# Kernel optimization log

Hardware: AMD Instinct MI355X
Metric: run time of the kernel (lower is better)

Reference implementation:

```python
import jax, jax.numpy as jnp
import numpy as np

FRAC_BITS = 16            # fixed-point fractional bits (MPC fixedpoint precision)
SCALE = float(1 << FRAC_BITS)

def fxp(v):
    """Emulate dup_with_precision: round value to the fixed-point grid with
    FRAC_BITS fractional bits. Straight-through (identity) gradient, matching
    the MPC backward pass which propagates gradients through truncation."""
    return v + jax.lax.stop_gradient(jnp.round(v * SCALE) / SCALE - v)


def setup_inputs() -> dict:
    key = jax.random.key(0)
    kx, kw = jax.random.split(key)
    in_dim, out_dim, batch = 4096, 4096, 2048
    x = jax.random.normal(kx, (batch, in_dim), dtype=jnp.float32)
    # Dense_Local init: w ~ N(0, 1/sqrt(in_dim+1)), b = zeros
    w = jax.random.normal(kw, (in_dim, out_dim), dtype=jnp.float32) / np.sqrt(in_dim + 1)
    b = jnp.zeros((out_dim,), dtype=jnp.float32)
    return {"x": x, "w": w, "b": b}


def reference(x, w, b):
    # quantize operands to the fixed-point grid (values live on the grid in MPC)
    xq = fxp(x)
    wq = fxp(w)
    # y = x @ w, then dup_with_precision(x.fixedpoint): truncate product back
    y = fxp(jnp.matmul(xq, wq))           # [batch, out_dim]
    # + bias
    y = y + fxp(b)
    # secure ReLU: s = drelu_local(y) (sign bit), y = relu(y, s) = y * s
    s = y >= 0
    y = jnp.where(s, y, jnp.zeros((), dtype=y.dtype))
    # final dup_with_precision(new_fixedpoint=x.fixedpoint)
    return fxp(y)
```

## Files before the change

kernel.cpp:

```cpp
#include <hip/hip_runtime.h>
#include <hip/hip_bf16.h>
#include <stdint.h>

#define M_DIM 2048
#define N_DIM 4096
#define K_DIM 4096

#define NT 64

typedef short short8 __attribute__((ext_vector_type(8)));
typedef float f32x4 __attribute__((ext_vector_type(4)));

typedef __attribute__((address_space(1))) unsigned int gu32;
typedef __attribute__((address_space(3))) unsigned int lu32;

__device__ static inline unsigned short f32_to_bf16(float f) {
  union { float f; unsigned int u; } v; v.f = f;
  unsigned int u = v.u;
  u += 0x7FFFu + ((u >> 16) & 1u);
  return (unsigned short)(u >> 16);
}

__global__ void cvt_x_kernel(const float* __restrict__ in, unsigned short* __restrict__ out) {
  size_t i = ((size_t)blockIdx.x * blockDim.x + threadIdx.x) * 8;
  f32x4 a = *(const f32x4*)(in + i);
  f32x4 b = *(const f32x4*)(in + i + 4);
  short8 o;
  o[0] = (short)f32_to_bf16(a[0]); o[1] = (short)f32_to_bf16(a[1]);
  o[2] = (short)f32_to_bf16(a[2]); o[3] = (short)f32_to_bf16(a[3]);
  o[4] = (short)f32_to_bf16(b[0]); o[5] = (short)f32_to_bf16(b[1]);
  o[6] = (short)f32_to_bf16(b[2]); o[7] = (short)f32_to_bf16(b[3]);
  *(short8*)(out + i) = o;
}

__global__ void transpose_cvt_w_kernel(const float* __restrict__ w, unsigned short* __restrict__ wt) {
  __shared__ unsigned short tile[64][64 + 8];
  int bn = blockIdx.x * 64;
  int bk = blockIdx.y * 64;
  int t = threadIdx.x;
  int c4 = (t & 15) * 4;
  int r0 = t >> 4;
#pragma unroll
  for (int p = 0; p < 4; ++p) {
    int r = r0 + p * 16;
    f32x4 v = *(const f32x4*)(w + (size_t)(bk + r) * N_DIM + bn + c4);
    tile[c4 + 0][r] = f32_to_bf16(v[0]);
    tile[c4 + 1][r] = f32_to_bf16(v[1]);
    tile[c4 + 2][r] = f32_to_bf16(v[2]);
    tile[c4 + 3][r] = f32_to_bf16(v[3]);
  }
  __syncthreads();
  int orow = t >> 2;
  int oc = (t & 3) * 16;
  short8 lo, hi;
#pragma unroll
  for (int j = 0; j < 8; ++j) {
    lo[j] = (short)tile[orow][oc + j];
    hi[j] = (short)tile[orow][oc + 8 + j];
  }
  unsigned short* op = wt + (size_t)(bn + orow) * K_DIM + bk + oc;
  *(short8*)(op) = lo;
  *(short8*)(op + 8) = hi;
}


__global__ __launch_bounds__(256, 1) void gemm4_kernel(
    const unsigned short* __restrict__ A, const unsigned short* __restrict__ Bt,
    const float* __restrict__ bias, float* __restrict__ C) {
  __shared__ unsigned short smA[3 * 24576];
  char* smemc = (char*)&smA[0];

  const int tid = threadIdx.x;
  const int lane = tid & 63;
  const int w = tid >> 6;
  const int wm = w >> 1, wn = w & 1;

  const int id = blockIdx.x;
  const int x = id & 7, j = id >> 3;
  const int by = ((x >> 2) << 3) + (j >> 2);
  const int bx = ((x & 3) << 2) + (j & 3);
  const int r0 = by * 128, c0 = bx * 256;

  const int l8 = lane >> 3, l7 = lane & 7;
  const int chunkE = ((l7 ^ l8) << 3);
  const unsigned short* Ag = A + (size_t)(r0 + w * 32 + l8) * K_DIM + chunkE;
  const unsigned short* Bg = Bt + (size_t)(c0 + w * 64 + l8) * K_DIM + chunkE;

#define GL(gp, ldsoff) __builtin_amdgcn_global_load_lds((gu32*)(gp), (lu32*)(smemc + (ldsoff)), 16, 0, 0)
  auto STAGE = [&](int T, int sb) {
#pragma unroll
    for (int i = 0; i < 4; ++i)
      GL(Ag + (size_t)T * 64 + (size_t)i * 8 * K_DIM, sb + w * 4096 + i * 1024);
#pragma unroll
    for (int i = 0; i < 8; ++i)
      GL(Bg + (size_t)T * 64 + (size_t)i * 8 * K_DIM, sb + 16384 + w * 8192 + i * 1024);
  };

  const int l15 = lane & 15, hi = lane >> 4;
  const int aR = (wm * 64 + l15) * 64;
  const int bR = 8192 + (wn * 128 + l15) * 64;
  const int slot0 = ((hi ^ l7) << 3);
  const int slot1 = (((4 + hi) ^ l7) << 3);

  f32x4 acc[4][8] = {};

  STAGE(0, 0);
  STAGE(1, 49152);

  int cs = 0;
  for (int t = 0; t < NT; ++t) {
    const int sE = cs * 24576;
    const int stB = (cs == 0 ? 2 : cs - 1) * 49152;

    if (t < NT - 1) asm volatile("s_waitcnt vmcnt(12) lgkmcnt(0)" ::: "memory");
    else            asm volatile("s_waitcnt vmcnt(0) lgkmcnt(0)" ::: "memory");
    __builtin_amdgcn_sched_barrier(0);
    asm volatile("s_barrier" ::: "memory");

    short8 a0[4], b0[8];
#pragma unroll
    for (int m = 0; m < 4; ++m) a0[m] = *(const short8*)(smA + sE + aR + m * 1024 + slot0);
#pragma unroll
    for (int n = 0; n < 8; ++n) b0[n] = *(const short8*)(smA + sE + bR + n * 1024 + slot0);
    if (t + 2 < NT) STAGE(t + 2, stB);

    __builtin_amdgcn_s_setprio(1);
#pragma unroll
    for (int m = 0; m < 4; ++m)
#pragma unroll
      for (int n = 0; n < 8; ++n)
        acc[m][n] = __builtin_amdgcn_mfma_f32_16x16x32_bf16(a0[m], b0[n], acc[m][n], 0, 0, 0);
    __builtin_amdgcn_s_setprio(0);

    short8 a1[4], b1[8];
#pragma unroll
    for (int m = 0; m < 4; ++m) a1[m] = *(const short8*)(smA + sE + aR + m * 1024 + slot1);
#pragma unroll
    for (int n = 0; n < 8; ++n) b1[n] = *(const short8*)(smA + sE + bR + n * 1024 + slot1);

    __builtin_amdgcn_s_setprio(1);
#pragma unroll
    for (int m = 0; m < 4; ++m)
#pragma unroll
      for (int n = 0; n < 8; ++n)
        acc[m][n] = __builtin_amdgcn_mfma_f32_16x16x32_bf16(a1[m], b1[n], acc[m][n], 0, 0, 0);
    __builtin_amdgcn_s_setprio(0);

    cs = (cs == 2) ? 0 : cs + 1;
  }

  const float S = 65536.0f, IS = 1.0f / 65536.0f;
  const int lr = hi * 4;
#pragma unroll
  for (int n = 0; n < 8; ++n) {
    int gcol = c0 + wn * 128 + n * 16 + l15;
    float bq = rintf(bias[gcol] * S) * IS;
#pragma unroll
    for (int m = 0; m < 4; ++m) {
      int grow = r0 + wm * 64 + m * 16 + lr;
      float* outp = C + (size_t)grow * N_DIM + gcol;
#pragma unroll
      for (int r = 0; r < 4; ++r) {
        float t = rintf(acc[m][n][r] * S) * IS + bq;
        t = t > 0.0f ? t : 0.0f;
        outp[(size_t)r * N_DIM] = t;
      }
    }
  }
#undef GL
}

__global__ __launch_bounds__(256, 2) void gemm_fb_kernel(
    const float* __restrict__ Xf, const float* __restrict__ Wf,
    const float* __restrict__ bias, float* __restrict__ C) {
  __shared__ unsigned short As[128][64];
  __shared__ unsigned short Bs[128][64];
  int tid = threadIdx.x;
  int lane = tid & 63;
  int wid = tid >> 6;
  int wr = wid >> 1, wc = wid & 1;
  int r0 = blockIdx.y * 128;
  int c0 = blockIdx.x * 128;
  f32x4 acc[4][4] = {};
  for (int kt = 0; kt < K_DIM / 64; ++kt) {
    __syncthreads();
    int ar = tid >> 1;
    int ac = (tid & 1) * 32;
    const float* xp = Xf + (size_t)(r0 + ar) * K_DIM + kt * 64 + ac;
#pragma unroll
    for (int jj = 0; jj < 8; ++jj) {
      f32x4 v = *(const f32x4*)(xp + jj * 4);
      As[ar][ac + jj * 4 + 0] = f32_to_bf16(v[0]);
      As[ar][ac + jj * 4 + 1] = f32_to_bf16(v[1]);
      As[ar][ac + jj * 4 + 2] = f32_to_bf16(v[2]);
      As[ar][ac + jj * 4 + 3] = f32_to_bf16(v[3]);
    }
    int bk_ = tid >> 2;
    int bc = (tid & 3) * 32;
    const float* wp = Wf + (size_t)(kt * 64 + bk_) * N_DIM + c0 + bc;
#pragma unroll
    for (int jj = 0; jj < 8; ++jj) {
      f32x4 v = *(const f32x4*)(wp + jj * 4);
      Bs[bc + jj * 4 + 0][bk_] = f32_to_bf16(v[0]);
      Bs[bc + jj * 4 + 1][bk_] = f32_to_bf16(v[1]);
      Bs[bc + jj * 4 + 2][bk_] = f32_to_bf16(v[2]);
      Bs[bc + jj * 4 + 3][bk_] = f32_to_bf16(v[3]);
    }
    __syncthreads();
#pragma unroll
    for (int ks = 0; ks < 2; ++ks) {
      int co = ks * 32 + (lane >> 4) * 8;
      int rA = wr * 64 + (lane & 15);
      int rB = wc * 64 + (lane & 15);
      short8 a[4], b[4];
#pragma unroll
      for (int m = 0; m < 4; ++m) a[m] = *(const short8*)&As[rA + m * 16][co];
#pragma unroll
      for (int n = 0; n < 4; ++n) b[n] = *(const short8*)&Bs[rB + n * 16][co];
#pragma unroll
      for (int m = 0; m < 4; ++m)
#pragma unroll
        for (int n = 0; n < 4; ++n)
          acc[m][n] = __builtin_amdgcn_mfma_f32_16x16x32_bf16(a[m], b[n], acc[m][n], 0, 0, 0);
    }
  }
  const float S = 65536.0f, IS = 1.0f / 65536.0f;
  int lr = (lane >> 4) * 4;
  int lc = lane & 15;
#pragma unroll
  for (int n = 0; n < 4; ++n) {
    int gcol = c0 + wc * 64 + n * 16 + lc;
    float bq = rintf(bias[gcol] * S) * IS;
#pragma unroll
    for (int m = 0; m < 4; ++m) {
      int grow = r0 + wr * 64 + m * 16 + lr;
      float* outp = C + (size_t)grow * N_DIM + gcol;
#pragma unroll
      for (int r = 0; r < 4; ++r) {
        float t = rintf(acc[m][n][r] * S) * IS + bq;
        t = t > 0.0f ? t : 0.0f;
        outp[(size_t)r * N_DIM] = t;
      }
    }
  }
}

extern "C" void kernel_launch(void* const* d_in, const int* in_sizes, int n_in,
                              void* d_out, int out_size, void* d_ws, size_t ws_size,
                              hipStream_t stream) {
  const float* x = (const float*)d_in[0];
  const float* w = (const float*)d_in[1];
  const float* b = (const float*)d_in[2];
  float* out = (float*)d_out;

  size_t needA = (size_t)M_DIM * K_DIM * sizeof(unsigned short);
  size_t needB = (size_t)K_DIM * N_DIM * sizeof(unsigned short);

  if (ws_size >= needA + needB) {
    unsigned short* Abf = (unsigned short*)d_ws;
    unsigned short* Btbf = (unsigned short*)((char*)d_ws + needA);
    cvt_x_kernel<<<(M_DIM * (size_t)K_DIM / 8 + 255) / 256, 256, 0, stream>>>(x, Abf);
    transpose_cvt_w_kernel<<<dim3(N_DIM / 64, K_DIM / 64), 256, 0, stream>>>(w, Btbf);
    gemm4_kernel<<<256, 256, 0, stream>>>(Abf, Btbf, b, out);
  } else {
    gemm_fb_kernel<<<dim3(N_DIM / 128, M_DIM / 128), 256, 0, stream>>>(x, w, b, out);
  }
}
```

Baseline: 95.81 us.

## Shrink GEMM tile to 128x128 with double buffering and 512 blocks

Replaces the 128x256 tile, triple-buffered GEMM (256 blocks, one per CU) with a 128x128 tile, double-buffered variant launched as 512 blocks. The next K-slice prefetch is now issued right after the barrier, with a full vmcnt(0) wait each iteration. The block-to-XCD mapping is adjusted for the new grid. The aim is more blocks per CU and lower register and LDS pressure for better occupancy, at the cost of lower per-block data reuse and a shallower prefetch pipeline.

```diff
diff --git a/kernel.cpp b/kernel.cpp
--- a/kernel.cpp
+++ b/kernel.cpp
@@ -64,11 +64,11 @@
 }
 
 
-__global__ __launch_bounds__(256, 1) void gemm4_kernel(
+__global__ __launch_bounds__(256) void gemm2b_kernel(
     const unsigned short* __restrict__ A, const unsigned short* __restrict__ Bt,
     const float* __restrict__ bias, float* __restrict__ C) {
-  __shared__ unsigned short smA[3 * 24576];
-  char* smemc = (char*)&smA[0];
+  __shared__ unsigned short sm[2 * 16384];
+  char* smemc = (char*)&sm[0];
 
   const int tid = threadIdx.x;
   const int lane = tid & 63;
@@ -76,84 +76,82 @@
   const int wm = w >> 1, wn = w & 1;
 
   const int id = blockIdx.x;
-  const int x = id & 7, j = id >> 3;
-  const int by = ((x >> 2) << 3) + (j >> 2);
-  const int bx = ((x & 3) << 2) + (j & 3);
-  const int r0 = by * 128, c0 = bx * 256;
+  const int xcd = id & 7, j = id >> 3;
+  const int by = ((xcd >> 2) << 3) + (j >> 3);
+  const int bx = ((xcd & 3) << 3) + (j & 7);
+  const int r0 = by * 128, c0 = bx * 128;
 
   const int l8 = lane >> 3, l7 = lane & 7;
   const int chunkE = ((l7 ^ l8) << 3);
   const unsigned short* Ag = A + (size_t)(r0 + w * 32 + l8) * K_DIM + chunkE;
-  const unsigned short* Bg = Bt + (size_t)(c0 + w * 64 + l8) * K_DIM + chunkE;
+  const unsigned short* Bg = Bt + (size_t)(c0 + w * 32 + l8) * K_DIM + chunkE;
 
 #define GL(gp, ldsoff) __builtin_amdgcn_global_load_lds((gu32*)(gp), (lu32*)(smemc + (ldsoff)), 16, 0, 0)
-  auto STAGE = [&](int T, int sb) {
-#pragma unroll
-    for (int i = 0; i < 4; ++i)
-      GL(Ag + (size_t)T * 64 + (size_t)i * 8 * K_DIM, sb + w * 4096 + i * 1024);
-#pragma unroll
-    for (int i = 0; i < 8; ++i)
-      GL(Bg + (size_t)T * 64 + (size_t)i * 8 * K_DIM, sb + 16384 + w * 8192 + i * 1024);
-  };
+#define STAGE(T, sb)                                                        \
+  do {                                                                      \
+    _Pragma("unroll") for (int i = 0; i < 4; ++i)                           \
+        GL(Ag + (size_t)(T) * 64 + (size_t)i * 8 * K_DIM,                   \
+           (sb) + w * 4096 + i * 1024);                                     \
+    _Pragma("unroll") for (int i = 0; i < 4; ++i)                           \
+        GL(Bg + (size_t)(T) * 64 + (size_t)i * 8 * K_DIM,                   \
+           (sb) + 16384 + w * 4096 + i * 1024);                             \
+  } while (0)
 
   const int l15 = lane & 15, hi = lane >> 4;
   const int aR = (wm * 64 + l15) * 64;
-  const int bR = 8192 + (wn * 128 + l15) * 64;
+  const int bR = 8192 + (wn * 64 + l15) * 64;
   const int slot0 = ((hi ^ l7) << 3);
   const int slot1 = (((4 + hi) ^ l7) << 3);
 
-  f32x4 acc[4][8] = {};
+  f32x4 acc[4][4] = {};
 
   STAGE(0, 0);
-  STAGE(1, 49152);
 
   int cs = 0;
   for (int t = 0; t < NT; ++t) {
-    const int sE = cs * 24576;
-    const int stB = (cs == 0 ? 2 : cs - 1) * 49152;
-
-    if (t < NT - 1) asm volatile("s_waitcnt vmcnt(12) lgkmcnt(0)" ::: "memory");
-    else            asm volatile("s_waitcnt vmcnt(0) lgkmcnt(0)" ::: "memory");
+    const int sE = cs * 16384;
+    const int stB = (cs ^ 1) * 32768;
+
+    asm volatile("s_waitcnt vmcnt(0) lgkmcnt(0)" ::: "memory");
     __builtin_amdgcn_sched_barrier(0);
     asm volatile("s_barrier" ::: "memory");
 
-    short8 a0[4], b0[8];
-#pragma unroll
-    for (int m = 0; m < 4; ++m) a0[m] = *(const short8*)(smA + sE + aR + m * 1024 + slot0);
-#pragma unroll
-    for (int n = 0; n < 8; ++n) b0[n] = *(const short8*)(smA + sE + bR + n * 1024 + slot0);
-    if (t + 2 < NT) STAGE(t + 2, stB);
-
+    if (t + 1 < NT) STAGE(t + 1, stB);
+
+    short8 a0[4], b0[4];
+#pragma unroll
+    for (int m = 0; m < 4; ++m) a0[m] = *(const short8*)(sm + sE + aR + m * 1024 + slot0);
+#pragma unroll
+    for (int n = 0; n < 4; ++n) b0[n] = *(const short8*)(sm + sE + bR + n * 1024 + slot0);
     __builtin_amdgcn_s_setprio(1);
 #pragma unroll
     for (int m = 0; m < 4; ++m)
 #pragma unroll
-      for (int n = 0; n < 8; ++n)
+      for (int n = 0; n < 4; ++n)
         acc[m][n] = __builtin_amdgcn_mfma_f32_16x16x32_bf16(a0[m], b0[n], acc[m][n], 0, 0, 0);
     __builtin_amdgcn_s_setprio(0);
 
-    short8 a1[4], b1[8];
-#pragma unroll
-    for (int m = 0; m < 4; ++m) a1[m] = *(const short8*)(smA + sE + aR + m * 1024 + slot1);
-#pragma unroll
-    for (int n = 0; n < 8; ++n) b1[n] = *(const short8*)(smA + sE + bR + n * 1024 + slot1);
-
+    short8 a1[4], b1[4];
+#pragma unroll
+    for (int m = 0; m < 4; ++m) a1[m] = *(const short8*)(sm + sE + aR + m * 1024 + slot1);
+#pragma unroll
+    for (int n = 0; n < 4; ++n) b1[n] = *(const short8*)(sm + sE + bR + n * 1024 + slot1);
     __builtin_amdgcn_s_setprio(1);
 #pragma unroll
     for (int m = 0; m < 4; ++m)
 #pragma unroll
-      for (int n = 0; n < 8; ++n)
+      for (int n = 0; n < 4; ++n)
         acc[m][n] = __builtin_amdgcn_mfma_f32_16x16x32_bf16(a1[m], b1[n], acc[m][n], 0, 0, 0);
     __builtin_amdgcn_s_setprio(0);
 
-    cs = (cs == 2) ? 0 : cs + 1;
+    cs ^= 1;
   }
 
   const float S = 65536.0f, IS = 1.0f / 65536.0f;
   const int lr = hi * 4;
 #pragma unroll
-  for (int n = 0; n < 8; ++n) {
-    int gcol = c0 + wn * 128 + n * 16 + l15;
+  for (int n = 0; n < 4; ++n) {
+    int gcol = c0 + wn * 64 + n * 16 + l15;
     float bq = rintf(bias[gcol] * S) * IS;
 #pragma unroll
     for (int m = 0; m < 4; ++m) {
@@ -168,6 +166,7 @@
     }
   }
 #undef GL
+#undef STAGE
 }
 
 __global__ __launch_bounds__(256, 2) void gemm_fb_kernel(
@@ -261,7 +260,7 @@
     unsigned short* Btbf = (unsigned short*)((char*)d_ws + needA);
     cvt_x_kernel<<<(M_DIM * (size_t)K_DIM / 8 + 255) / 256, 256, 0, stream>>>(x, Abf);
     transpose_cvt_w_kernel<<<dim3(N_DIM / 64, K_DIM / 64), 256, 0, stream>>>(w, Btbf);
-    gemm4_kernel<<<256, 256, 0, stream>>>(Abf, Btbf, b, out);
+    gemm2b_kernel<<<512, 256, 0, stream>>>(Abf, Btbf, b, out);
   } else {
     gemm_fb_kernel<<<dim3(N_DIM / 128, M_DIM / 128), 256, 0, stream>>>(x, w, b, out);
   }
```

New measurement: 95.43 us. Within noise of the previous version (-0.4%).
